# Optimization experiments

Hardware: AMD Instinct MI355X
Metric: run time of the kernel (lower is better)

The kernel has to match this reference:

```python
import jax, jax.numpy as jnp
import numpy as np

E = 1.0
I = 1.0
P = 1.0
LENGTH = 1.0
N_POINTS = 2_000_000


def _mlp_scalar(x, W1, b1, W2, b2, W3, b3, W4, b4):
    # x: scalar. 1 -> 15 -> 15 -> 15 -> 1 tanh MLP (dropout inactive, training=False).
    h = jnp.tanh(x * W1[0] + b1)          # [15]
    h = jnp.tanh(h @ W2 + b2)             # [15]
    h = jnp.tanh(h @ W3 + b3)             # [15]
    return (h @ W4 + b4)[0]               # scalar w(x)


def _derivs(x_points, W1, b1, W2, b2, W3, b3, W4, b4):
    """Returns [w, w_x, w_xx, w_xxx, w_xxxx], each of shape [N, 1]."""
    f = lambda x: _mlp_scalar(x, W1, b1, W2, b2, W3, b3, W4, b4)
    d1 = jax.grad(f)
    d2 = jax.grad(d1)
    d3 = jax.grad(d2)
    d4 = jax.grad(d3)
    return [jax.vmap(g)(x_points)[:, None] for g in (f, d1, d2, d3, d4)]


def setup_inputs() -> dict:
    key = jax.random.key(0)
    ks = jax.random.split(key, 5)
    d = 15
    # Glorot-ish small init so tanh stays in its active range
    W1 = jax.random.normal(ks[0], (1, d), jnp.float32) * 0.5
    W2 = jax.random.normal(ks[1], (d, d), jnp.float32) * (1.0 / np.sqrt(d))
    W3 = jax.random.normal(ks[2], (d, d), jnp.float32) * (1.0 / np.sqrt(d))
    W4 = jax.random.normal(ks[3], (d, 1), jnp.float32) * (1.0 / np.sqrt(d))
    x = jax.random.uniform(ks[4], (N_POINTS,), jnp.float32) * LENGTH
    return {
        "x": x,
        "W1": W1, "b1": jnp.zeros((d,), jnp.float32),
        "W2": W2, "b2": jnp.zeros((d,), jnp.float32),
        "W3": W3, "b3": jnp.zeros((d,), jnp.float32),
        "W4": W4, "b4": jnp.zeros((1,), jnp.float32),
    }


def reference(x, W1, b1, W2, b2, W3, b3, W4, b4):
    params = (W1, b1, W2, b2, W3, b3, W4, b4)
    x_left = jnp.zeros_like(x)
    x_right = jnp.full_like(x, LENGTH)

    g_field = _derivs(x, *params)
    g_left = _derivs(x_left, *params)
    g_right = _derivs(x_right, *params)

    w_0, w_0_x = g_left[0], g_left[1]
    m_L = g_right[2]
    w_L = g_right[0]
    w_xxxx = g_field[4]

    pde_residual = w_xxxx + P / (E * I)            # [N,1]
    pde_loss = jnp.mean(jnp.square(pde_residual))  # scalar
    left_bc_w_loss = jnp.square(w_0)               # [N,1]
    left_bc_w_x_loss = jnp.square(w_0_x)           # [N,1]
    right_bc_M_loss = jnp.square(m_L)              # [N,1]
    right_bc_w_loss = jnp.square(w_L)              # [N,1]

    loss = pde_loss + left_bc_w_loss + left_bc_w_x_loss + right_bc_M_loss + right_bc_w_loss
    return (loss, pde_loss, left_bc_w_loss, left_bc_w_x_loss, right_bc_M_loss, right_bc_w_loss)
```

## Files before the change

### kernel.cpp

```cpp
#include <hip/hip_runtime.h>
#include <math.h>

#define DH 15
#define NNODES 64
#define M_DEG  63

typedef float v2f __attribute__((ext_vector_type(2)));

__device__ __forceinline__ void tanh_fs(float u0, float& t, float& s,
                                        float& f2, float& f3, float& f4) {
    float e = __builtin_amdgcn_exp2f(u0 * 2.885390081777927f);
    float r = __builtin_amdgcn_rcpf(1.0f + e);
    t = 1.0f - 2.0f * r;
    s = 4.0f * r * (1.0f - r);
    f2 = -2.0f * t * s;
    f3 = s * (4.0f * t * t - 2.0f * s);
    f4 = 8.0f * t * s * (2.0f * s - t * t);
}

__device__ __forceinline__ void tanh_jet(float u0, float u1, float u2,
                                         float u3, float u4, float h[5]) {
    float t, s, f2, f3, f4;
    tanh_fs(u0, t, s, f2, f3, f4);
    float u1s = u1 * u1;
    h[0] = t;
    h[1] = s * u1;
    h[2] = f2 * u1s + s * u2;
    h[3] = f3 * u1s * u1 + 3.0f * f2 * u1 * u2 + s * u3;
    h[4] = f4 * u1s * u1s + 6.0f * f3 * u1s * u2
         + f2 * (3.0f * u2 * u2 + 4.0f * u1 * u3) + s * u4;
}

__global__ void __launch_bounds__(256)
pinn_nodes(const float* __restrict__ W1, const float* __restrict__ b1,
           const float* __restrict__ W2, const float* __restrict__ b2,
           const float* __restrict__ W3, const float* __restrict__ b3,
           const float* __restrict__ W4, const float* __restrict__ b4,
           float* __restrict__ C, float* __restrict__ bc) {
    __shared__ float hs[DH][5][NNODES];
    __shared__ alignas(16) float rsh[NNODES];
    const int tid  = threadIdx.x;
    const int lane = tid & 63;
    const int wq   = tid >> 6;

    float xv;
    if (lane == 0)           xv = 1.0f;
    else if (lane == M_DEG)  xv = 0.0f;
    else xv = 0.5f + 0.5f * __builtin_amdgcn_cosf((float)lane * (1.0f / 126.0f));

#pragma unroll
    for (int jj = 0; jj < 4; ++jj) {
        int j = wq * 4 + jj;
        if (j < DH) {
            float w = W1[j];
            float t, s, f2, f3, f4;
            tanh_fs(fmaf(xv, w, b1[j]), t, s, f2, f3, f4);
            float w2 = w * w;
            hs[j][0][lane] = t;
            hs[j][1][lane] = s * w;
            hs[j][2][lane] = f2 * w2;
            hs[j][3][lane] = f3 * w2 * w;
            hs[j][4][lane] = f4 * w2 * w2;
        }
    }
    __syncthreads();

    const float* Ws[2] = {W2, W3};
    const float* Bs[2] = {b2, b3};
#pragma unroll
    for (int L = 0; L < 2; ++L) {
        const float* W = Ws[L];
        const float* B = Bs[L];
        float u[4][5];
#pragma unroll
        for (int jj = 0; jj < 4; ++jj)
#pragma unroll
            for (int c = 0; c < 5; ++c) u[jj][c] = 0.f;
#pragma unroll
        for (int k = 0; k < DH; ++k) {
            float g0 = hs[k][0][lane], g1 = hs[k][1][lane], g2 = hs[k][2][lane],
                  g3 = hs[k][3][lane], g4 = hs[k][4][lane];
#pragma unroll
            for (int jj = 0; jj < 4; ++jj) {
                int j = wq * 4 + jj;
                float w = (j < DH) ? W[k * DH + j] : 0.f;
                u[jj][0] = fmaf(g0, w, u[jj][0]);
                u[jj][1] = fmaf(g1, w, u[jj][1]);
                u[jj][2] = fmaf(g2, w, u[jj][2]);
                u[jj][3] = fmaf(g3, w, u[jj][3]);
                u[jj][4] = fmaf(g4, w, u[jj][4]);
            }
        }
        __syncthreads();
#pragma unroll
        for (int jj = 0; jj < 4; ++jj) {
            int j = wq * 4 + jj;
            if (j < DH) {
                float hj[5];
                tanh_jet(u[jj][0] + B[j], u[jj][1], u[jj][2], u[jj][3],
                         u[jj][4], hj);
                hs[j][0][lane] = hj[0]; hs[j][1][lane] = hj[1];
                hs[j][2][lane] = hj[2]; hs[j][3][lane] = hj[3];
                hs[j][4][lane] = hj[4];
            }
        }
        __syncthreads();
    }

    if (wq == 0) {
        float o0 = b4[0], o1 = 0.f, o2 = 0.f, o3 = 0.f, o4 = 0.f;
#pragma unroll
        for (int k = 0; k < DH; ++k) {
            float w = W4[k];
            o0 = fmaf(hs[k][0][lane], w, o0);
            o1 = fmaf(hs[k][1][lane], w, o1);
            o2 = fmaf(hs[k][2][lane], w, o2);
            o3 = fmaf(hs[k][3][lane], w, o3);
            o4 = fmaf(hs[k][4][lane], w, o4);
        }
        rsh[lane] = ((lane == 0 || lane == M_DEG) ? 0.5f : 1.0f) * (o4 + 1.0f);
        if (lane == M_DEG) {
            bc[0] = o0; bc[1] = o1; bc[2] = o2; bc[3] = o3; bc[4] = o4;
        }
        if (lane == 0) {
            bc[5] = o0; bc[6] = o1; bc[7] = o2; bc[8] = o3; bc[9] = o4;
        }
        __builtin_amdgcn_s_waitcnt(0);

        float rs[NNODES];
#pragma unroll
        for (int i = 0; i < NNODES / 4; ++i) {
            float4 q = *reinterpret_cast<const float4*>(&rsh[4 * i]);
            rs[4*i] = q.x; rs[4*i+1] = q.y; rs[4*i+2] = q.z; rs[4*i+3] = q.w;
        }
        float kstep = (float)lane * (1.0f / 126.0f);
        float ph = 0.f;
        float a0 = 0.f, a1 = 0.f, a2 = 0.f, a3 = 0.f;
#pragma unroll
        for (int jj = 0; jj < NNODES; ++jj) {
            float cv = __builtin_amdgcn_cosf(ph);
            ph += kstep;
            ph = (ph >= 1.0f) ? ph - 1.0f : ph;
            float v = rs[jj] * cv;
            if ((jj & 3) == 0) a0 += v;
            else if ((jj & 3) == 1) a1 += v;
            else if ((jj & 3) == 2) a2 += v;
            else a3 += v;
        }
        float e = ((a0 + a1) + (a2 + a3)) * (2.0f / 63.0f);
        if (lane == 0 || lane == M_DEG) e *= 0.5f;
        C[lane] = e;
    }
}

__device__ __forceinline__ void fill_region(float* __restrict__ p, float c,
                                            size_t n, size_t tid, size_t stride) {
    size_t head = ((16 - ((size_t)p & 15)) & 15) >> 2;
    if (head > n) head = n;
    if (tid < head) p[tid] = c;
    size_t n4 = (n - head) >> 2;
    float4* p4 = reinterpret_cast<float4*>(p + head);
    float4 cv = {c, c, c, c};
    for (size_t i = tid; i < n4; i += stride) p4[i] = cv;
    size_t t = head + (n4 << 2) + tid;
    if (t < n) p[t] = c;
}

__global__ void __launch_bounds__(256)
pinn_pde(const float* __restrict__ x, const float* __restrict__ Cc,
         const float* __restrict__ bc, float* __restrict__ out,
         double* __restrict__ partials, int N) {
    float e[NNODES];
#pragma unroll
    for (int k = 0; k < NNODES; ++k) e[k] = Cc[k];

    int tid = threadIdx.x;
    size_t gtid = (size_t)blockIdx.x * blockDim.x + tid;
    size_t gstride = (size_t)gridDim.x * blockDim.x;

    {
        float lbw  = bc[0] * bc[0];
        float lbwx = bc[1] * bc[1];
        float rbM  = bc[7] * bc[7];
        float rbw  = bc[5] * bc[5];
        fill_region(out + (size_t)1 * N + 1, lbw,  (size_t)N, gtid, gstride);
        fill_region(out + (size_t)2 * N + 1, lbwx, (size_t)N, gtid, gstride);
        fill_region(out + (size_t)3 * N + 1, rbM,  (size_t)N, gtid, gstride);
        fill_region(out + (size_t)4 * N + 1, rbw,  (size_t)N, gtid, gstride);
    }

    v2f accA = {0.f, 0.f}, accB = {0.f, 0.f};
    int i0 = (int)gtid;
    int gsz = (int)gstride;
    int n4 = N >> 2;
    const float4* x4 = reinterpret_cast<const float4*>(x);
    for (int i = i0; i < n4; i += gsz) {
        float4 xv = x4[i];
        v2f tA = {2.f * xv.x - 1.f, 2.f * xv.y - 1.f};
        v2f tB = {2.f * xv.z - 1.f, 2.f * xv.w - 1.f};
        v2f t2A = tA + tA, t2B = tB + tB;
        v2f b0A = {0.f, 0.f}, b1A = {0.f, 0.f};
        v2f b0B = {0.f, 0.f}, b1B = {0.f, 0.f};
#pragma unroll
        for (int k = M_DEG; k >= 1; --k) {
            v2f ek = {e[k], e[k]};
            v2f bnA = __builtin_elementwise_fma(t2A, b0A, ek) - b1A;
            b1A = b0A; b0A = bnA;
            v2f bnB = __builtin_elementwise_fma(t2B, b0B, ek) - b1B;
            b1B = b0B; b0B = bnB;
        }
        v2f e0 = {e[0], e[0]};
        v2f rA = __builtin_elementwise_fma(tA, b0A, e0) - b1A;
        v2f rB = __builtin_elementwise_fma(tB, b0B, e0) - b1B;
        accA = __builtin_elementwise_fma(rA, rA, accA);
        accB = __builtin_elementwise_fma(rB, rB, accB);
    }
    float accs = (accA.x + accA.y) + (accB.x + accB.y);
    for (int i = (n4 << 2) + i0; i < N; i += gsz) {
        float t = 2.f * x[i] - 1.f, t2 = t + t;
        float b0 = 0.f, b1 = 0.f;
#pragma unroll
        for (int k = M_DEG; k >= 1; --k) {
            float bn = fmaf(t2, b0, e[k]) - b1;
            b1 = b0; b0 = bn;
        }
        float r = fmaf(t, b0, e[0]) - b1;
        accs = fmaf(r, r, accs);
    }

    double a = (double)accs;
#pragma unroll
    for (int off = 32; off > 0; off >>= 1) a += __shfl_down(a, off, 64);
    __shared__ double red[4];
    int lane = tid & 63, wid = tid >> 6;
    if (lane == 0) red[wid] = a;
    __syncthreads();
    if (tid == 0) partials[blockIdx.x] = red[0] + red[1] + red[2] + red[3];
}

__global__ void __launch_bounds__(256)
pinn_finish(const double* __restrict__ partials, int nparts,
            const float* __restrict__ bc,
            float* __restrict__ out, int N, float* __restrict__ consts) {
    int tid = threadIdx.x;
    double a = 0.0;
    for (int i = tid; i < nparts; i += 256) a += partials[i];
#pragma unroll
    for (int off = 32; off > 0; off >>= 1) a += __shfl_down(a, off, 64);
    __shared__ double red[4];
    if ((tid & 63) == 0) red[tid >> 6] = a;
    __syncthreads();
    if (tid == 0) {
        double total = red[0] + red[1] + red[2] + red[3];
        float pdef = (float)(total / (double)N);
        float lbw  = bc[0] * bc[0];
        float lbwx = bc[1] * bc[1];
        float rbM  = bc[7] * bc[7];
        float rbw  = bc[5] * bc[5];
        float loss = pdef + lbw + lbwx + rbM + rbw;
        consts[0] = loss;
        out[N] = pdef;
    }
}

__global__ void __launch_bounds__(256)
pinn_fill_loss(float* __restrict__ out, const float* __restrict__ consts, int N) {
    float c = consts[0];
    size_t tid = (size_t)blockIdx.x * blockDim.x + threadIdx.x;
    size_t stride = (size_t)gridDim.x * blockDim.x;
    fill_region(out, c, (size_t)N, tid, stride);
}

extern "C" void kernel_launch(void* const* d_in, const int* in_sizes, int n_in,
                              void* d_out, int out_size, void* d_ws, size_t ws_size,
                              hipStream_t stream) {
    const float* x  = (const float*)d_in[0];
    const float* W1 = (const float*)d_in[1];
    const float* b1 = (const float*)d_in[2];
    const float* W2 = (const float*)d_in[3];
    const float* b2 = (const float*)d_in[4];
    const float* W3 = (const float*)d_in[5];
    const float* b3 = (const float*)d_in[6];
    const float* W4 = (const float*)d_in[7];
    const float* b4 = (const float*)d_in[8];
    float* out = (float*)d_out;
    int N = in_sizes[0];

    float*  C        = (float*)d_ws;
    float*  bc       = (float*)((char*)d_ws + 256);
    float*  consts   = (float*)((char*)d_ws + 384);
    double* partials = (double*)((char*)d_ws + 1024);

    int NB = 512;
    size_t need = 1024 + (size_t)NB * 8;
    if (ws_size < need) {
        NB = (int)((ws_size > 1024 + 8) ? (ws_size - 1024) / 8 : 1);
        if (NB < 1) NB = 1;
        if (NB > 512) NB = 512;
    }

    hipLaunchKernelGGL(pinn_nodes, dim3(1), dim3(256), 0, stream,
                       W1, b1, W2, b2, W3, b3, W4, b4, C, bc);
    hipLaunchKernelGGL(pinn_pde, dim3(NB), dim3(256), 0, stream,
                       x, C, bc, out, partials, N);
    hipLaunchKernelGGL(pinn_finish, dim3(1), dim3(256), 0, stream,
                       partials, NB, bc, out, N, consts);
    int gx = (N / 4 + 255) / 256;
    if (gx > 1024) gx = 1024;
    if (gx < 1) gx = 1;
    hipLaunchKernelGGL(pinn_fill_loss, dim3(gx), dim3(256), 0, stream,
                       out, consts, N);
}
```

Measured before the change: 31.87 us.

## Fuse node fitting into PDE kernel and merge finish with loss fill

Every block of the main kernel now recomputes the 64-node MLP jet and the Chebyshev coefficients itself, keeping them in LDS. This removes the separate single-block nodes launch and its serialization. The final reduction is folded into the loss-fill kernel: each block re-reduces the partials and writes the broadcast loss, which removes another launch. The cost is redundant per-block node work (tanh jets plus a 64x64 cosine transform) and a repeated reduction of partials in every fill block.

```diff
diff --git a/kernel.cpp b/kernel.cpp
--- a/kernel.cpp
+++ b/kernel.cpp
@@ -31,14 +31,31 @@
          + f2 * (3.0f * u2 * u2 + 4.0f * u1 * u3) + s * u4;
 }
 
+__device__ __forceinline__ void fill_region(float* __restrict__ p, float c,
+                                            size_t n, size_t tid, size_t stride) {
+    size_t head = ((16 - ((size_t)p & 15)) & 15) >> 2;
+    if (head > n) head = n;
+    if (tid < head) p[tid] = c;
+    size_t n4 = (n - head) >> 2;
+    float4* p4 = reinterpret_cast<float4*>(p + head);
+    float4 cv = {c, c, c, c};
+    for (size_t i = tid; i < n4; i += stride) p4[i] = cv;
+    size_t t = head + (n4 << 2) + tid;
+    if (t < n) p[t] = c;
+}
+
 __global__ void __launch_bounds__(256)
-pinn_nodes(const float* __restrict__ W1, const float* __restrict__ b1,
-           const float* __restrict__ W2, const float* __restrict__ b2,
-           const float* __restrict__ W3, const float* __restrict__ b3,
-           const float* __restrict__ W4, const float* __restrict__ b4,
-           float* __restrict__ C, float* __restrict__ bc) {
+pinn_main(const float* __restrict__ x,
+          const float* __restrict__ W1, const float* __restrict__ b1,
+          const float* __restrict__ W2, const float* __restrict__ b2,
+          const float* __restrict__ W3, const float* __restrict__ b3,
+          const float* __restrict__ W4, const float* __restrict__ b4,
+          float* __restrict__ out, float* __restrict__ bcg,
+          double* __restrict__ partials, int N) {
     __shared__ float hs[DH][5][NNODES];
     __shared__ alignas(16) float rsh[NNODES];
+    __shared__ float C_lds[NNODES];
+    __shared__ float bc_lds[10];
     const int tid  = threadIdx.x;
     const int lane = tid & 63;
     const int wq   = tid >> 6;
@@ -120,10 +137,18 @@
         }
         rsh[lane] = ((lane == 0 || lane == M_DEG) ? 0.5f : 1.0f) * (o4 + 1.0f);
         if (lane == M_DEG) {
-            bc[0] = o0; bc[1] = o1; bc[2] = o2; bc[3] = o3; bc[4] = o4;
+            bc_lds[0] = o0; bc_lds[1] = o1; bc_lds[2] = o2;
+            bc_lds[3] = o3; bc_lds[4] = o4;
+            if (blockIdx.x == 0) {
+                bcg[0] = o0; bcg[1] = o1; bcg[2] = o2; bcg[3] = o3; bcg[4] = o4;
+            }
         }
         if (lane == 0) {
-            bc[5] = o0; bc[6] = o1; bc[7] = o2; bc[8] = o3; bc[9] = o4;
+            bc_lds[5] = o0; bc_lds[6] = o1; bc_lds[7] = o2;
+            bc_lds[8] = o3; bc_lds[9] = o4;
+            if (blockIdx.x == 0) {
+                bcg[5] = o0; bcg[6] = o1; bcg[7] = o2; bcg[8] = o3; bcg[9] = o4;
+            }
         }
         __builtin_amdgcn_s_waitcnt(0);
 
@@ -149,45 +174,28 @@
         }
         float e = ((a0 + a1) + (a2 + a3)) * (2.0f / 63.0f);
         if (lane == 0 || lane == M_DEG) e *= 0.5f;
-        C[lane] = e;
-    }
-}
-
-__device__ __forceinline__ void fill_region(float* __restrict__ p, float c,
-                                            size_t n, size_t tid, size_t stride) {
-    size_t head = ((16 - ((size_t)p & 15)) & 15) >> 2;
-    if (head > n) head = n;
-    if (tid < head) p[tid] = c;
-    size_t n4 = (n - head) >> 2;
-    float4* p4 = reinterpret_cast<float4*>(p + head);
-    float4 cv = {c, c, c, c};
-    for (size_t i = tid; i < n4; i += stride) p4[i] = cv;
-    size_t t = head + (n4 << 2) + tid;
-    if (t < n) p[t] = c;
-}
-
-__global__ void __launch_bounds__(256)
-pinn_pde(const float* __restrict__ x, const float* __restrict__ Cc,
-         const float* __restrict__ bc, float* __restrict__ out,
-         double* __restrict__ partials, int N) {
+        C_lds[lane] = e;
+    }
+    __syncthreads();
+
+    float lbw  = bc_lds[0] * bc_lds[0];
+    float lbwx = bc_lds[1] * bc_lds[1];
+    float rbM  = bc_lds[7] * bc_lds[7];
+    float rbw  = bc_lds[5] * bc_lds[5];
     float e[NNODES];
 #pragma unroll
-    for (int k = 0; k < NNODES; ++k) e[k] = Cc[k];
-
-    int tid = threadIdx.x;
+    for (int k = 0; k < NNODES; ++k) {
+        int bits = __builtin_amdgcn_readfirstlane(__float_as_int(C_lds[k]));
+        e[k] = __int_as_float(bits);
+    }
+
     size_t gtid = (size_t)blockIdx.x * blockDim.x + tid;
     size_t gstride = (size_t)gridDim.x * blockDim.x;
 
-    {
-        float lbw  = bc[0] * bc[0];
-        float lbwx = bc[1] * bc[1];
-        float rbM  = bc[7] * bc[7];
-        float rbw  = bc[5] * bc[5];
-        fill_region(out + (size_t)1 * N + 1, lbw,  (size_t)N, gtid, gstride);
-        fill_region(out + (size_t)2 * N + 1, lbwx, (size_t)N, gtid, gstride);
-        fill_region(out + (size_t)3 * N + 1, rbM,  (size_t)N, gtid, gstride);
-        fill_region(out + (size_t)4 * N + 1, rbw,  (size_t)N, gtid, gstride);
-    }
+    fill_region(out + (size_t)1 * N + 1, lbw,  (size_t)N, gtid, gstride);
+    fill_region(out + (size_t)2 * N + 1, lbwx, (size_t)N, gtid, gstride);
+    fill_region(out + (size_t)3 * N + 1, rbM,  (size_t)N, gtid, gstride);
+    fill_region(out + (size_t)4 * N + 1, rbw,  (size_t)N, gtid, gstride);
 
     v2f accA = {0.f, 0.f}, accB = {0.f, 0.f};
     int i0 = (int)gtid;
@@ -195,9 +203,9 @@
     int n4 = N >> 2;
     const float4* x4 = reinterpret_cast<const float4*>(x);
     for (int i = i0; i < n4; i += gsz) {
-        float4 xv = x4[i];
-        v2f tA = {2.f * xv.x - 1.f, 2.f * xv.y - 1.f};
-        v2f tB = {2.f * xv.z - 1.f, 2.f * xv.w - 1.f};
+        float4 xv4 = x4[i];
+        v2f tA = {2.f * xv4.x - 1.f, 2.f * xv4.y - 1.f};
+        v2f tB = {2.f * xv4.z - 1.f, 2.f * xv4.w - 1.f};
         v2f t2A = tA + tA, t2B = tB + tB;
         v2f b0A = {0.f, 0.f}, b1A = {0.f, 0.f};
         v2f b0B = {0.f, 0.f}, b1B = {0.f, 0.f};
@@ -232,16 +240,14 @@
 #pragma unroll
     for (int off = 32; off > 0; off >>= 1) a += __shfl_down(a, off, 64);
     __shared__ double red[4];
-    int lane = tid & 63, wid = tid >> 6;
-    if (lane == 0) red[wid] = a;
+    if ((tid & 63) == 0) red[tid >> 6] = a;
     __syncthreads();
     if (tid == 0) partials[blockIdx.x] = red[0] + red[1] + red[2] + red[3];
 }
 
 __global__ void __launch_bounds__(256)
-pinn_finish(const double* __restrict__ partials, int nparts,
-            const float* __restrict__ bc,
-            float* __restrict__ out, int N, float* __restrict__ consts) {
+pinn_loss(const double* __restrict__ partials, int nparts,
+          const float* __restrict__ bc, float* __restrict__ out, int N) {
     int tid = threadIdx.x;
     double a = 0.0;
     for (int i = tid; i < nparts; i += 256) a += partials[i];
@@ -250,25 +256,18 @@
     __shared__ double red[4];
     if ((tid & 63) == 0) red[tid >> 6] = a;
     __syncthreads();
-    if (tid == 0) {
-        double total = red[0] + red[1] + red[2] + red[3];
-        float pdef = (float)(total / (double)N);
-        float lbw  = bc[0] * bc[0];
-        float lbwx = bc[1] * bc[1];
-        float rbM  = bc[7] * bc[7];
-        float rbw  = bc[5] * bc[5];
-        float loss = pdef + lbw + lbwx + rbM + rbw;
-        consts[0] = loss;
-        out[N] = pdef;
-    }
-}
-
-__global__ void __launch_bounds__(256)
-pinn_fill_loss(float* __restrict__ out, const float* __restrict__ consts, int N) {
-    float c = consts[0];
-    size_t tid = (size_t)blockIdx.x * blockDim.x + threadIdx.x;
-    size_t stride = (size_t)gridDim.x * blockDim.x;
-    fill_region(out, c, (size_t)N, tid, stride);
+    double total = red[0] + red[1] + red[2] + red[3];
+    float pdef = (float)(total / (double)N);
+    float lbw  = bc[0] * bc[0];
+    float lbwx = bc[1] * bc[1];
+    float rbM  = bc[7] * bc[7];
+    float rbw  = bc[5] * bc[5];
+    float loss = pdef + lbw + lbwx + rbM + rbw;
+
+    size_t gtid = (size_t)blockIdx.x * blockDim.x + tid;
+    size_t gstride = (size_t)gridDim.x * blockDim.x;
+    fill_region(out, loss, (size_t)N, gtid, gstride);
+    if (blockIdx.x == 0 && tid == 0) out[N] = pdef;
 }
 
 extern "C" void kernel_launch(void* const* d_in, const int* in_sizes, int n_in,
@@ -286,9 +285,7 @@
     float* out = (float*)d_out;
     int N = in_sizes[0];
 
-    float*  C        = (float*)d_ws;
     float*  bc       = (float*)((char*)d_ws + 256);
-    float*  consts   = (float*)((char*)d_ws + 384);
     double* partials = (double*)((char*)d_ws + 1024);
 
     int NB = 512;
@@ -299,15 +296,12 @@
         if (NB > 512) NB = 512;
     }
 
-    hipLaunchKernelGGL(pinn_nodes, dim3(1), dim3(256), 0, stream,
-                       W1, b1, W2, b2, W3, b3, W4, b4, C, bc);
-    hipLaunchKernelGGL(pinn_pde, dim3(NB), dim3(256), 0, stream,
-                       x, C, bc, out, partials, N);
-    hipLaunchKernelGGL(pinn_finish, dim3(1), dim3(256), 0, stream,
-                       partials, NB, bc, out, N, consts);
+    hipLaunchKernelGGL(pinn_main, dim3(NB), dim3(256), 0, stream,
+                       x, W1, b1, W2, b2, W3, b3, W4, b4,
+                       out, bc, partials, N);
     int gx = (N / 4 + 255) / 256;
-    if (gx > 1024) gx = 1024;
+    if (gx > 512) gx = 512;
     if (gx < 1) gx = 1;
-    hipLaunchKernelGGL(pinn_fill_loss, dim3(gx), dim3(256), 0, stream,
-                       out, consts, N);
-}
+    hipLaunchKernelGGL(pinn_loss, dim3(gx), dim3(256), 0, stream,
+                       partials, NB, bc, out, N);
+}
```

After: 29.56 us. 7.3% less time.
